# Kernel tuning notes

Measured on AMD Instinct MI355X. Metric: run time of the kernel, lower is better.

Reference implementation:

```python
import jax, jax.numpy as jnp
import numpy as np

N = 50000        # nodes
E = 800000       # edges (avg degree 16)
D_IN = 19        # in_channels(16) + 2 coords + 1 observed flag
H = 64           # graph_hidden
L = 3            # graph_layers
EPS = 1e-5       # BatchNorm eps


def setup_inputs() -> dict:
    key = jax.random.key(0)
    ks = jax.random.split(key, 12)
    s = 0.05
    x = jax.random.normal(ks[0], (N, D_IN), jnp.float32)
    edge_index = jax.random.randint(ks[1], (2, E), 0, N, dtype=jnp.int32)
    return {
        "x": x,
        "edge_index": edge_index,
        # input projection + input BN
        "w_in": jax.random.normal(ks[2], (D_IN, H), jnp.float32) * s,
        "b_in": jnp.zeros((H,), jnp.float32),
        "bn0_g": jnp.ones((H,), jnp.float32),
        "bn0_b": jnp.zeros((H,), jnp.float32),
        # per-layer SAGEConv: lin_l (aggregated neighbors, with bias), lin_r (self, no bias)
        "wl": jax.random.normal(ks[3], (L, H, H), jnp.float32) * s,
        "bl": jnp.zeros((L, H), jnp.float32),
        "wr": jax.random.normal(ks[4], (L, H, H), jnp.float32) * s,
        # per-layer BatchNorm affine
        "bn_g": jnp.ones((L, H), jnp.float32),
        "bn_b": jnp.zeros((L, H), jnp.float32),
    }


def _batchnorm(h, g, b):
    # training-mode BN over the node axis (biased variance, like torch)
    mu = h.mean(axis=0)
    var = h.var(axis=0)
    return (h - mu) * jax.lax.rsqrt(var + EPS) * g + b


def reference(x, edge_index, w_in, b_in, bn0_g, bn0_b, wl, bl, wr, bn_g, bn_b):
    src = edge_index[0]
    dst = edge_index[1]
    n = x.shape[0]

    # input_proj -> BN -> ReLU  (dropout is identity at inference)
    h = x @ w_in + b_in
    h = jax.nn.relu(_batchnorm(h, bn0_g, bn0_b))

    # in-degree for mean aggregation (computed once)
    deg = jax.ops.segment_sum(jnp.ones((src.shape[0],), h.dtype), dst, num_segments=n)
    denom = jnp.maximum(deg, 1.0)[:, None]

    for l in range(L):
        # SAGEConv(mean): gather source feats, segment-mean into targets
        msgs = h[src]                                        # [E, H] gather
        agg = jax.ops.segment_sum(msgs, dst, num_segments=n) / denom
        h_new = agg @ wl[l] + bl[l] + h @ wr[l]
        h_new = jax.nn.relu(_batchnorm(h_new, bn_g[l], bn_b[l]))
        h = h + h_new                                        # residual
    return h
```

## Files before the change

### kernel.cpp

```cpp
#include <hip/hip_runtime.h>
#include <hip/hip_bf16.h>

#define NODES 50000
#define EDGES 800000
#define DIN   19
#define LAYERS 3
#define BN_EPS 1e-5f

#define NBINS 196
#define EPB   4096
#define NBLK  196
#define NTILES 782
#define TPB   256

typedef __attribute__((ext_vector_type(4))) float f32x4;
typedef __attribute__((ext_vector_type(2))) float f32x2;
typedef __attribute__((ext_vector_type(8))) short s16x8;

__device__ inline ushort bf16bits(float f) {
    __hip_bfloat16 h = __float2bfloat16(f);
    return *reinterpret_cast<ushort*>(&h);
}

#if __has_builtin(__builtin_amdgcn_cvt_pk_f32_fp8) && __has_builtin(__builtin_amdgcn_cvt_pk_fp8_f32)
__device__ inline unsigned pack4_fp8(float a, float b, float c, float d) {
    unsigned w = __builtin_amdgcn_cvt_pk_fp8_f32(a, b, 0u, false);
    return __builtin_amdgcn_cvt_pk_fp8_f32(c, d, w, true);
}
__device__ inline void acc4_fp8(unsigned v, float& a0, float& a1, float& a2, float& a3) {
    f32x2 lo = __builtin_amdgcn_cvt_pk_f32_fp8(v, false);
    f32x2 hi = __builtin_amdgcn_cvt_pk_f32_fp8(v, true);
    a0 += lo.x; a1 += lo.y; a2 += hi.x; a3 += hi.y;
}
#else
__device__ inline unsigned enc1(float f) {
    _Float16 hf = (_Float16)f;
    unsigned u = (unsigned)*reinterpret_cast<unsigned short*>(&hf);
    u = (u + 0x7Fu + ((u >> 8) & 1u)) >> 8;
    return u & 0xFFu;
}
__device__ inline float dec1(unsigned b) {
    unsigned short u = (unsigned short)(b << 8);
    _Float16 hf = *reinterpret_cast<_Float16*>(&u);
    return (float)hf;
}
__device__ inline unsigned pack4_fp8(float a, float b, float c, float d) {
    return enc1(a) | (enc1(b) << 8) | (enc1(c) << 16) | (enc1(d) << 24);
}
__device__ inline void acc4_fp8(unsigned v, float& a0, float& a1, float& a2, float& a3) {
    a0 += dec1(v & 0xFF); a1 += dec1((v >> 8) & 0xFF);
    a2 += dec1((v >> 16) & 0xFF); a3 += dec1(v >> 24);
}
#endif


__global__ void k_wprep(const float* __restrict__ w_in, const float* __restrict__ wl,
                        const float* __restrict__ wr, ushort* __restrict__ WiT,
                        ushort* __restrict__ WcatT, int* __restrict__ bintot,
                        float* __restrict__ stats) {
    int i0 = blockIdx.x * blockDim.x + threadIdx.x;
    int stride = gridDim.x * blockDim.x;
    for (int i = i0; i < NBINS; i += stride) bintot[i] = 0;
    for (int i = i0; i < 4 * 2048; i += stride) stats[i] = 0.0f;
    for (int i = i0; i < 64 * 32; i += stride) {
        int c = i >> 5, k = i & 31;
        WiT[i] = bf16bits(k < DIN ? w_in[k * 64 + c] : 0.0f);
    }
    for (int i = i0; i < LAYERS * 64 * 128; i += stride) {
        int l = i >> 13, rem = i & 8191;
        int c = rem >> 7, k = rem & 127;
        float v = (k < 64) ? wl[(l * 64 + k) * 64 + c] : wr[(l * 64 + (k - 64)) * 64 + c];
        WcatT[i] = bf16bits(v);
    }
}


__global__ __launch_bounds__(1024) void k_sortA(const int* __restrict__ src, const int* __restrict__ dst,
                                                int2* __restrict__ cb, int* __restrict__ bintot,
                                                unsigned* __restrict__ bbuf) {
    __shared__ int hist[256];
    __shared__ int cur[256];
    __shared__ int wsum4[4];
    __shared__ unsigned stage[EPB];
    int blk = blockIdx.x, t = threadIdx.x;
    int e0 = blk * EPB;
    int ne = min(EPB, EDGES - e0);
    int d[4]; unsigned pk[4];
    #pragma unroll
    for (int i = 0; i < 4; ++i) {
        int j = t + i * 1024;
        if (j < ne) {
            int dd = dst[e0 + j];
            d[i] = dd;
            pk[i] = ((unsigned)(dd & 255) << 24) | (unsigned)src[e0 + j];
        } else d[i] = -1;
    }
    if (t < 256) hist[t] = 0;
    __syncthreads();
    #pragma unroll
    for (int i = 0; i < 4; ++i)
        if (d[i] >= 0) atomicAdd(&hist[d[i] >> 8], 1);
    __syncthreads();
    int ln = t & 63, wv = t >> 6;
    int cntv = 0, inc = 0;
    if (t < 256) {
        cntv = hist[t];
        inc = cntv;
        #pragma unroll
        for (int s = 1; s < 64; s <<= 1) {
            int u = __shfl_up(inc, s);
            if (ln >= s) inc += u;
        }
        if (ln == 63) wsum4[wv] = inc;
    }
    __syncthreads();
    if (t < 256) {
        int woff = 0;
        #pragma unroll
        for (int i = 0; i < 4; ++i) if (i < wv) woff += wsum4[i];
        int excl = woff + inc - cntv;
        cur[t] = excl;
        if (t < NBINS) {
            cb[t * NBLK + blk] = make_int2(excl, cntv);
            if (cntv) atomicAdd(&bintot[t], cntv);
        }
    }
    __syncthreads();
    #pragma unroll
    for (int i = 0; i < 4; ++i)
        if (d[i] >= 0) {
            int slot = atomicAdd(&cur[d[i] >> 8], 1);
            stage[slot] = pk[i];
        }
    __syncthreads();
    #pragma unroll
    for (int i = 0; i < 4; ++i) {
        int j = t + i * 1024;
        if (j < ne) bbuf[e0 + j] = stage[j];
    }
}


__device__ inline int ubound(const int* pre, int f) {
    int lo = 0, hi = NBLK;
    while (lo + 1 < hi) {
        int mid = (lo + hi) >> 1;
        if (pre[mid] <= f) lo = mid; else hi = mid;
    }
    return lo;
}

__global__ __launch_bounds__(TPB) void k_binB(const int2* __restrict__ cb, const int* __restrict__ bintot,
                                              const unsigned* __restrict__ bbuf,
                                              int* __restrict__ off, float* __restrict__ rden,
                                              int* __restrict__ ebuf) {
    __shared__ int red[256];
    __shared__ int segoff[NBLK], segcnt[NBLK], pre[NBLK + 1];
    __shared__ int deg[256], loff[256], cur[256];
    __shared__ int wsum4[4];
    int b = blockIdx.x, t = threadIdx.x;
    int ln = t & 63, wv = t >> 6;
    red[t] = (t < b) ? bintot[t] : 0;
    __syncthreads();
    #pragma unroll
    for (int s = 128; s > 0; s >>= 1) {
        if (t < s) red[t] += red[t + s];
        __syncthreads();
    }
    int binoff = red[0];
    if (t < NBLK) {
        int2 c = cb[b * NBLK + t];
        segoff[t] = c.x; segcnt[t] = c.y;
    }
    deg[t] = 0; cur[t] = 0;
    __syncthreads();
    if (wv == 0) {
        int carry = 0;
        for (int base = 0; base < NBLK; base += 64) {
            int idx = base + ln;
            int v = (idx < NBLK) ? segcnt[idx] : 0;
            int inc = v;
            #pragma unroll
            for (int s = 1; s < 64; s <<= 1) {
                int u = __shfl_up(inc, s);
                if (ln >= s) inc += u;
            }
            if (idx < NBLK) pre[idx] = carry + inc - v;
            carry += __shfl(inc, 63);
        }
        if (ln == 0) pre[NBLK] = carry;
    }
    __syncthreads();
    int total = pre[NBLK];
    for (int f = t; f < total; f += TPB) {
        int sg = ubound(pre, f);
        unsigned e = bbuf[sg * EPB + segoff[sg] + (f - pre[sg])];
        atomicAdd(&deg[e >> 24], 1);
    }
    __syncthreads();
    int dv = deg[t], inc2 = dv;
    #pragma unroll
    for (int s = 1; s < 64; s <<= 1) {
        int u = __shfl_up(inc2, s);
        if (ln >= s) inc2 += u;
    }
    if (ln == 63) wsum4[wv] = inc2;
    __syncthreads();
    int woff = 0;
    #pragma unroll
    for (int i = 0; i < 4; ++i) if (i < wv) woff += wsum4[i];
    int excl = woff + inc2 - dv;
    loff[t] = excl;
    int node = (b << 8) + t;
    if (node < NODES) {
        off[node] = binoff + excl;
        rden[node] = 1.0f / fmaxf((float)dv, 1.0f);
    }
    if (b == NBINS - 1 && t == 0) off[NODES] = EDGES;
    __syncthreads();
    for (int f = t; f < total; f += TPB) {
        int sg = ubound(pre, f);
        unsigned e = bbuf[sg * EPB + segoff[sg] + (f - pre[sg])];
        int dd = e >> 24;
        int slot = atomicAdd(&cur[dd], 1);
        ebuf[binoff + loff[dd] + slot] = (int)(e & 0xFFFFFFu);
    }
}


__device__ inline void gemm_epilogue(int t, int row0, f32x4* acc, const float* __restrict__ bias,
                                     ushort* __restrict__ tb, float* __restrict__ stats,
                                     float (*red)[128]) {
    int lane = t & 63, wave = t >> 6;
    int r = lane & 15, g = lane >> 4;
    float s_[4], q_[4];
    #pragma unroll
    for (int j = 0; j < 4; ++j) {
        float b = bias[j * 16 + r];
        float s = 0.0f, q = 0.0f;
        #pragma unroll
        for (int i = 0; i < 4; ++i) {
            int row = row0 + wave * 16 + g * 4 + i;
            if (row < NODES) {
                float v = acc[j][i] + b;
                tb[(size_t)row * 64 + j * 16 + r] = bf16bits(v);
                s += v; q += v * v;
            }
        }
        s += __shfl_xor(s, 16); s += __shfl_xor(s, 32);
        q += __shfl_xor(q, 16); q += __shfl_xor(q, 32);
        s_[j] = s; q_[j] = q;
    }
    if (g == 0) {
        #pragma unroll
        for (int j = 0; j < 4; ++j) {
            red[wave][j * 16 + r] = s_[j];
            red[wave][64 + j * 16 + r] = q_[j];
        }
    }
    __syncthreads();
    if (t < 128) {
        float tot = red[0][t] + red[1][t] + red[2][t] + red[3][t];
        atomicAdd(&stats[t * 16], tot);
    }
}


__global__ __launch_bounds__(TPB) void k_gemm0(const float* __restrict__ x, const ushort* __restrict__ WiT,
                                               const float* __restrict__ bias, ushort* __restrict__ tb,
                                               float* __restrict__ stats) {
    __shared__ ushort xt[64][40];
    __shared__ float red[4][128];
    int t = threadIdx.x, rb = blockIdx.x;
    int row0 = rb * 64;
    int nv = min(64, NODES - row0);
    unsigned* xz = (unsigned*)xt;
    for (int i = t; i < 64 * 20; i += TPB) xz[i] = 0;
    __syncthreads();
    const float* xs = x + (size_t)row0 * DIN;
    for (int e = t; e < nv * DIN; e += TPB) {
        int n = e / DIN, k = e - n * DIN;
        xt[n][k] = bf16bits(xs[e]);
    }
    __syncthreads();
    int lane = t & 63, wave = t >> 6;
    int r = lane & 15, g = lane >> 4;
    f32x4 acc[4] = {{0.f,0.f,0.f,0.f},{0.f,0.f,0.f,0.f},{0.f,0.f,0.f,0.f},{0.f,0.f,0.f,0.f}};
    s16x8 af = *(const s16x8*)&xt[wave * 16 + r][g * 8];
    #pragma unroll
    for (int j = 0; j < 4; ++j) {
        s16x8 bf = *(const s16x8*)(WiT + (size_t)(j * 16 + r) * 32 + g * 8);
        acc[j] = __builtin_amdgcn_mfma_f32_16x16x32_bf16(af, bf, acc[j], 0, 0, 0);
    }
    gemm_epilogue(t, row0, acc, bias, tb, stats, red);
}


__global__ __launch_bounds__(TPB) void k_gemm(const ushort* __restrict__ AB, const ushort* __restrict__ WT,
                                              const float* __restrict__ bias, ushort* __restrict__ tb,
                                              float* __restrict__ stats) {
    __shared__ float red[4][128];
    int t = threadIdx.x;
    int lane = t & 63, wave = t >> 6;
    int row0 = blockIdx.x * 64;
    int r = lane & 15, g = lane >> 4;
    f32x4 acc[4] = {{0.f,0.f,0.f,0.f},{0.f,0.f,0.f,0.f},{0.f,0.f,0.f,0.f},{0.f,0.f,0.f,0.f}};
    int ar = row0 + wave * 16 + r;
    if (ar >= NODES) ar = NODES - 1;
    #pragma unroll
    for (int k0 = 0; k0 < 128; k0 += 32) {
        s16x8 af = *(const s16x8*)(AB + (size_t)ar * 128 + k0 + g * 8);
        #pragma unroll
        for (int j = 0; j < 4; ++j) {
            s16x8 bf = *(const s16x8*)(WT + (size_t)(j * 16 + r) * 128 + k0 + g * 8);
            acc[j] = __builtin_amdgcn_mfma_f32_16x16x32_bf16(af, bf, acc[j], 0, 0, 0);
        }
    }
    gemm_epilogue(t, row0, acc, bias, tb, stats, red);
}


__global__ void k_apply(const ushort* __restrict__ tb, const float* __restrict__ stats,
                        const float* __restrict__ gamma, const float* __restrict__ beta,
                        float* __restrict__ h, ushort* __restrict__ AB,
                        unsigned* __restrict__ hb8, int residual, int write_next) {
    int idx0 = blockIdx.x * blockDim.x + threadIdx.x;
    int stride = gridDim.x * blockDim.x;
    const float invN = 1.0f / NODES;
    for (int idx = idx0; idx < NODES * 16; idx += stride) {
        int n = idx >> 4;
        int j = (idx & 15) * 4;
        ushort4 tv = *(const ushort4*)(tb + (size_t)n * 64 + j);
        float tf[4] = { __uint_as_float((unsigned)tv.x << 16), __uint_as_float((unsigned)tv.y << 16),
                        __uint_as_float((unsigned)tv.z << 16), __uint_as_float((unsigned)tv.w << 16) };
        f32x4 hv;
        if (residual) hv = *(const f32x4*)(h + (size_t)n * 64 + j);
        float out[4];
        ushort ub[4];
        #pragma unroll
        for (int k = 0; k < 4; ++k) {
            int f = j + k;
            float mu = stats[f * 16] * invN;
            float var = stats[(64 + f) * 16] * invN - mu * mu;
            float sc = gamma[f] * rsqrtf(var + BN_EPS);
            float sh = beta[f] - mu * sc;
            float v = fmaxf(tf[k] * sc + sh, 0.0f);
            out[k] = residual ? (hv[k] + v) : v;
            ub[k] = bf16bits(out[k]);
        }
        *(f32x4*)(h + (size_t)n * 64 + j) = f32x4{out[0], out[1], out[2], out[3]};
        if (write_next) {
            *(ushort4*)(AB + (size_t)n * 128 + 64 + j) = make_ushort4(ub[0], ub[1], ub[2], ub[3]);
            hb8[(size_t)n * 16 + (idx & 15)] = pack4_fp8(out[0], out[1], out[2], out[3]);
        }
    }
}


__global__ void k_agg(const int* __restrict__ off, const int* __restrict__ ebuf,
                      const float* __restrict__ rden, const unsigned* __restrict__ hb8,
                      ushort* __restrict__ ABh) {
    unsigned* AB = (unsigned*)ABh;
    int t = threadIdx.x;
    int lane = t & 63;
    int q = lane >> 4;
    int fl = lane & 15;
    int w = blockIdx.x * (blockDim.x >> 6) + (t >> 6);
    int nw = gridDim.x * (blockDim.x >> 6);
    for (int n = w; n < NODES; n += nw) {
        int p0 = off[n], p1 = off[n + 1];
        float a0 = 0.f, a1 = 0.f, a2 = 0.f, a3 = 0.f;
        int p = p0 + q;
        for (; p + 12 < p1; p += 16) {
            int s0 = ebuf[p], s1 = ebuf[p + 4], s2 = ebuf[p + 8], s3 = ebuf[p + 12];
            unsigned v0 = hb8[(size_t)s0 * 16 + fl];
            unsigned v1 = hb8[(size_t)s1 * 16 + fl];
            unsigned v2 = hb8[(size_t)s2 * 16 + fl];
            unsigned v3 = hb8[(size_t)s3 * 16 + fl];
            acc4_fp8(v0, a0, a1, a2, a3);
            acc4_fp8(v1, a0, a1, a2, a3);
            acc4_fp8(v2, a0, a1, a2, a3);
            acc4_fp8(v3, a0, a1, a2, a3);
        }
        for (; p < p1; p += 4) {
            unsigned v = hb8[(size_t)ebuf[p] * 16 + fl];
            acc4_fp8(v, a0, a1, a2, a3);
        }
        a0 += __shfl_xor(a0, 16); a0 += __shfl_xor(a0, 32);
        a1 += __shfl_xor(a1, 16); a1 += __shfl_xor(a1, 32);
        a2 += __shfl_xor(a2, 16); a2 += __shfl_xor(a2, 32);
        a3 += __shfl_xor(a3, 16); a3 += __shfl_xor(a3, 32);
        if (q == 0) {
            float rd = rden[n];
            uint2 o;
            o.x = (unsigned)bf16bits(a0 * rd) | ((unsigned)bf16bits(a1 * rd) << 16);
            o.y = (unsigned)bf16bits(a2 * rd) | ((unsigned)bf16bits(a3 * rd) << 16);
            *(uint2*)(AB + (size_t)n * 64 + fl * 2) = o;
        }
    }
}


extern "C" void kernel_launch(void* const* d_in, const int* in_sizes, int n_in,
                              void* d_out, int out_size, void* d_ws, size_t ws_size,
                              hipStream_t stream) {
    const float* x    = (const float*)d_in[0];
    const int*   ei   = (const int*)d_in[1];
    const float* w_in = (const float*)d_in[2];
    const float* b_in = (const float*)d_in[3];
    const float* bn0g = (const float*)d_in[4];
    const float* bn0b = (const float*)d_in[5];
    const float* wl   = (const float*)d_in[6];
    const float* bl   = (const float*)d_in[7];
    const float* wr   = (const float*)d_in[8];
    const float* bng  = (const float*)d_in[9];
    const float* bnb  = (const float*)d_in[10];
    const int* esrc = ei;
    const int* edst = ei + EDGES;
    float* h = (float*)d_out;

    char* p = (char*)d_ws;
    auto alloc = [&](size_t bytes) {
        char* r = p;
        p += (bytes + 255) & ~size_t(255);
        return r;
    };
    int*      bintot = (int*)alloc((size_t)NBINS * 4);
    float*    stats  = (float*)alloc((size_t)4 * 2048 * 4);
    int2*     cb     = (int2*)alloc((size_t)NBINS * NBLK * 8);
    unsigned* bbuf   = (unsigned*)alloc((size_t)NBLK * EPB * 4);
    int*      off    = (int*)alloc((size_t)(NODES + 1) * 4);
    float*    rden   = (float*)alloc((size_t)NODES * 4);
    int*      ebuf   = (int*)alloc((size_t)EDGES * 4);
    ushort*   WiT    = (ushort*)alloc(64 * 32 * 2);
    ushort*   WcatT  = (ushort*)alloc(LAYERS * 64 * 128 * 2);
    ushort*   tb     = (ushort*)alloc((size_t)NODES * 64 * 2);
    ushort*   AB     = (ushort*)alloc((size_t)NODES * 128 * 2);
    unsigned* hb8    = (unsigned*)alloc((size_t)NODES * 16 * 4);

    k_wprep<<<128, TPB, 0, stream>>>(w_in, wl, wr, WiT, WcatT, bintot, stats);
    k_sortA<<<NBLK, 1024, 0, stream>>>(esrc, edst, cb, bintot, bbuf);
    k_binB<<<NBINS, TPB, 0, stream>>>(cb, bintot, bbuf, off, rden, ebuf);

    k_gemm0<<<NTILES, TPB, 0, stream>>>(x, WiT, b_in, tb, stats);
    k_apply<<<2048, TPB, 0, stream>>>(tb, stats, bn0g, bn0b, h, AB, hb8, 0, 1);

    for (int l = 0; l < LAYERS; ++l) {
        k_agg<<<2048, TPB, 0, stream>>>(off, ebuf, rden, hb8, AB);
        k_gemm<<<NTILES, TPB, 0, stream>>>(AB, WcatT + l * 8192, bl + l * 64,
                                           tb, stats + (l + 1) * 2048);
        k_apply<<<2048, TPB, 0, stream>>>(tb, stats + (l + 1) * 2048, bng + l * 64, bnb + l * 64,
                                          h, AB, hb8, 1, l < LAYERS - 1 ? 1 : 0);
    }
}
```

Before: 295.2 us.

## Co-schedule edge sort with input GEMM and CSR build with BN0 apply

```diff
diff --git a/kernel.cpp b/kernel.cpp
--- a/kernel.cpp
+++ b/kernel.cpp
@@ -11,6 +11,8 @@
 #define EPB   4096
 #define NBLK  196
 #define NTILES 782
+#define G0TILES 196
+#define APPLY_BLOCKS 2048
 #define TPB   256
 
 typedef __attribute__((ext_vector_type(4))) float f32x4;
@@ -54,10 +56,10 @@
 #endif
 
 
-__global__ void k_wprep(const float* __restrict__ w_in, const float* __restrict__ wl,
-                        const float* __restrict__ wr, ushort* __restrict__ WiT,
-                        ushort* __restrict__ WcatT, int* __restrict__ bintot,
-                        float* __restrict__ stats) {
+__global__ void k_prep(const float* __restrict__ w_in, const float* __restrict__ wl,
+                       const float* __restrict__ wr, ushort* __restrict__ WiT,
+                       ushort* __restrict__ WcatT, int* __restrict__ bintot,
+                       float* __restrict__ stats) {
     int i0 = blockIdx.x * blockDim.x + threadIdx.x;
     int stride = gridDim.x * blockDim.x;
     for (int i = i0; i < NBINS; i += stride) bintot[i] = 0;
@@ -75,14 +77,15 @@
 }
 
 
-__global__ __launch_bounds__(1024) void k_sortA(const int* __restrict__ src, const int* __restrict__ dst,
-                                                int2* __restrict__ cb, int* __restrict__ bintot,
-                                                unsigned* __restrict__ bbuf) {
-    __shared__ int hist[256];
-    __shared__ int cur[256];
-    __shared__ int wsum4[4];
-    __shared__ unsigned stage[EPB];
-    int blk = blockIdx.x, t = threadIdx.x;
+union SMemK2 {
+    struct { int hist[256], cur[256], wsum[4]; unsigned stage[EPB]; } sort;
+    struct { ushort xt[256][40]; float red[4][4][128]; } g0;
+};
+
+__device__ inline void do_sortA(int blk, int t, const int* __restrict__ src,
+                                const int* __restrict__ dst, int2* __restrict__ cb,
+                                int* __restrict__ bintot, unsigned* __restrict__ bbuf,
+                                SMemK2& sm) {
     int e0 = blk * EPB;
     int ne = min(EPB, EDGES - e0);
     int d[4]; unsigned pk[4];
@@ -95,31 +98,31 @@
             pk[i] = ((unsigned)(dd & 255) << 24) | (unsigned)src[e0 + j];
         } else d[i] = -1;
     }
-    if (t < 256) hist[t] = 0;
+    if (t < 256) sm.sort.hist[t] = 0;
     __syncthreads();
     #pragma unroll
     for (int i = 0; i < 4; ++i)
-        if (d[i] >= 0) atomicAdd(&hist[d[i] >> 8], 1);
+        if (d[i] >= 0) atomicAdd(&sm.sort.hist[d[i] >> 8], 1);
     __syncthreads();
     int ln = t & 63, wv = t >> 6;
     int cntv = 0, inc = 0;
     if (t < 256) {
-        cntv = hist[t];
+        cntv = sm.sort.hist[t];
         inc = cntv;
         #pragma unroll
         for (int s = 1; s < 64; s <<= 1) {
             int u = __shfl_up(inc, s);
             if (ln >= s) inc += u;
         }
-        if (ln == 63) wsum4[wv] = inc;
+        if (ln == 63) sm.sort.wsum[wv] = inc;
     }
     __syncthreads();
     if (t < 256) {
         int woff = 0;
         #pragma unroll
-        for (int i = 0; i < 4; ++i) if (i < wv) woff += wsum4[i];
+        for (int i = 0; i < 4; ++i) if (i < wv) woff += sm.sort.wsum[i];
         int excl = woff + inc - cntv;
-        cur[t] = excl;
+        sm.sort.cur[t] = excl;
         if (t < NBINS) {
             cb[t * NBLK + blk] = make_int2(excl, cntv);
             if (cntv) atomicAdd(&bintot[t], cntv);
@@ -129,15 +132,86 @@
     #pragma unroll
     for (int i = 0; i < 4; ++i)
         if (d[i] >= 0) {
-            int slot = atomicAdd(&cur[d[i] >> 8], 1);
-            stage[slot] = pk[i];
+            int slot = atomicAdd(&sm.sort.cur[d[i] >> 8], 1);
+            sm.sort.stage[slot] = pk[i];
         }
     __syncthreads();
     #pragma unroll
     for (int i = 0; i < 4; ++i) {
         int j = t + i * 1024;
-        if (j < ne) bbuf[e0 + j] = stage[j];
-    }
+        if (j < ne) bbuf[e0 + j] = sm.sort.stage[j];
+    }
+}
+
+__device__ inline void do_gemm0(int tile, int t, const float* __restrict__ x,
+                                const ushort* __restrict__ WiT, const float* __restrict__ bias,
+                                ushort* __restrict__ tb, float* __restrict__ stats,
+                                SMemK2& sm) {
+    int base = tile * 256;
+    int nv = min(256, NODES - base);
+    unsigned* xz = (unsigned*)sm.g0.xt;
+    for (int i = t; i < 256 * 20; i += 1024) xz[i] = 0;
+    __syncthreads();
+    const float* xs = x + (size_t)base * DIN;
+    for (int e = t; e < nv * DIN; e += 1024) {
+        int n = e / DIN, k = e - n * DIN;
+        sm.g0.xt[n][k] = bf16bits(xs[e]);
+    }
+    __syncthreads();
+    int grp = t >> 8, tl = t & 255;
+    int lane = t & 63, wl = (tl >> 6);
+    int r = lane & 15, g = lane >> 4;
+    f32x4 acc[4] = {{0.f,0.f,0.f,0.f},{0.f,0.f,0.f,0.f},{0.f,0.f,0.f,0.f},{0.f,0.f,0.f,0.f}};
+    s16x8 af = *(const s16x8*)&sm.g0.xt[grp * 64 + wl * 16 + r][g * 8];
+    #pragma unroll
+    for (int j = 0; j < 4; ++j) {
+        s16x8 bf = *(const s16x8*)(WiT + (size_t)(j * 16 + r) * 32 + g * 8);
+        acc[j] = __builtin_amdgcn_mfma_f32_16x16x32_bf16(af, bf, acc[j], 0, 0, 0);
+    }
+    int row0 = base + grp * 64 + wl * 16;
+    float s_[4], q_[4];
+    #pragma unroll
+    for (int j = 0; j < 4; ++j) {
+        float b = bias[j * 16 + r];
+        float s = 0.0f, q = 0.0f;
+        #pragma unroll
+        for (int i = 0; i < 4; ++i) {
+            int row = row0 + g * 4 + i;
+            if (row < NODES) {
+                float v = acc[j][i] + b;
+                tb[(size_t)row * 64 + j * 16 + r] = bf16bits(v);
+                s += v; q += v * v;
+            }
+        }
+        s += __shfl_xor(s, 16); s += __shfl_xor(s, 32);
+        q += __shfl_xor(q, 16); q += __shfl_xor(q, 32);
+        s_[j] = s; q_[j] = q;
+    }
+    if (g == 0) {
+        #pragma unroll
+        for (int j = 0; j < 4; ++j) {
+            sm.g0.red[grp][wl][j * 16 + r] = s_[j];
+            sm.g0.red[grp][wl][64 + j * 16 + r] = q_[j];
+        }
+    }
+    __syncthreads();
+    if (tl < 128) {
+        float tot = sm.g0.red[grp][0][tl] + sm.g0.red[grp][1][tl] +
+                    sm.g0.red[grp][2][tl] + sm.g0.red[grp][3][tl];
+        atomicAdd(&stats[tl * 16], tot);
+    }
+}
+
+__global__ __launch_bounds__(1024) void k_sort_g0(const int* __restrict__ esrc, const int* __restrict__ edst,
+                                                  int2* __restrict__ cb, int* __restrict__ bintot,
+                                                  unsigned* __restrict__ bbuf,
+                                                  const float* __restrict__ x, const ushort* __restrict__ WiT,
+                                                  const float* __restrict__ bias, ushort* __restrict__ tb,
+                                                  float* __restrict__ stats) {
+    __shared__ SMemK2 sm;
+    int t = threadIdx.x;
+    if (blockIdx.x < NBLK) do_sortA(blockIdx.x, t, esrc, edst, cb, bintot, bbuf, sm);
+    else                   do_gemm0(blockIdx.x - NBLK, t, x, WiT, bias, tb, stats, sm);
 }
 
 
@@ -150,67 +224,69 @@
     return lo;
 }
 
-__global__ __launch_bounds__(TPB) void k_binB(const int2* __restrict__ cb, const int* __restrict__ bintot,
-                                              const unsigned* __restrict__ bbuf,
-                                              int* __restrict__ off, float* __restrict__ rden,
-                                              int* __restrict__ ebuf) {
-    __shared__ int red[256];
-    __shared__ int segoff[NBLK], segcnt[NBLK], pre[NBLK + 1];
-    __shared__ int deg[256], loff[256], cur[256];
-    __shared__ int wsum4[4];
-    int b = blockIdx.x, t = threadIdx.x;
+struct SMemBinB {
+    int red[256];
+    int segoff[NBLK], segcnt[NBLK], pre[NBLK + 1];
+    int deg[256], loff[256], cur[256];
+    int wsum4[4];
+};
+
+__device__ inline void do_binB(int b, int t, const int2* __restrict__ cb,
+                               const int* __restrict__ bintot, const unsigned* __restrict__ bbuf,
+                               int* __restrict__ off, float* __restrict__ rden,
+                               int* __restrict__ ebuf, SMemBinB& sm) {
     int ln = t & 63, wv = t >> 6;
-    red[t] = (t < b) ? bintot[t] : 0;
+    sm.red[t] = (t < b) ? bintot[t] : 0;
     __syncthreads();
     #pragma unroll
     for (int s = 128; s > 0; s >>= 1) {
-        if (t < s) red[t] += red[t + s];
+        if (t < s) sm.red[t] += sm.red[t + s];
         __syncthreads();
     }
-    int binoff = red[0];
+    int binoff = sm.red[0];
     if (t < NBLK) {
         int2 c = cb[b * NBLK + t];
-        segoff[t] = c.x; segcnt[t] = c.y;
-    }
-    deg[t] = 0; cur[t] = 0;
+        sm.segoff[t] = c.x; sm.segcnt[t] = c.y;
+    }
+    sm.deg[t] = 0; sm.cur[t] = 0;
     __syncthreads();
     if (wv == 0) {
         int carry = 0;
         for (int base = 0; base < NBLK; base += 64) {
             int idx = base + ln;
-            int v = (idx < NBLK) ? segcnt[idx] : 0;
+            int v = (idx < NBLK) ? sm.segcnt[idx] : 0;
             int inc = v;
             #pragma unroll
             for (int s = 1; s < 64; s <<= 1) {
                 int u = __shfl_up(inc, s);
                 if (ln >= s) inc += u;
             }
-            if (idx < NBLK) pre[idx] = carry + inc - v;
+            if (idx < NBLK) sm.pre[idx] = carry + inc - v;
             carry += __shfl(inc, 63);
         }
-        if (ln == 0) pre[NBLK] = carry;
-    }
-    __syncthreads();
-    int total = pre[NBLK];
+        if (ln == 0) sm.pre[NBLK] = carry;
+    }
+    __syncthreads();
+    int total = sm.pre[NBLK];
     for (int f = t; f < total; f += TPB) {
-        int sg = ubound(pre, f);
-        unsigned e = bbuf[sg * EPB + segoff[sg] + (f - pre[sg])];
-        atomicAdd(&deg[e >> 24], 1);
-    }
-    __syncthreads();
-    int dv = deg[t], inc2 = dv;
+        int sg = ubound(sm.pre, f);
+        unsigned e = bbuf[sg * EPB + sm.segoff[sg] + (f - sm.pre[sg])];
+        atomicAdd(&sm.deg[e >> 24], 1);
+    }
+    __syncthreads();
+    int dv = sm.deg[t], inc2 = dv;
     #pragma unroll
     for (int s = 1; s < 64; s <<= 1) {
         int u = __shfl_up(inc2, s);
         if (ln >= s) inc2 += u;
     }
-    if (ln == 63) wsum4[wv] = inc2;
+    if (ln == 63) sm.wsum4[wv] = inc2;
     __syncthreads();
     int woff = 0;
     #pragma unroll
-    for (int i = 0; i < 4; ++i) if (i < wv) woff += wsum4[i];
+    for (int i = 0; i < 4; ++i) if (i < wv) woff += sm.wsum4[i];
     int excl = woff + inc2 - dv;
-    loff[t] = excl;
+    sm.loff[t] = excl;
     int node = (b << 8) + t;
     if (node < NODES) {
         off[node] = binoff + excl;
@@ -219,80 +295,65 @@
     if (b == NBINS - 1 && t == 0) off[NODES] = EDGES;
     __syncthreads();
     for (int f = t; f < total; f += TPB) {
-        int sg = ubound(pre, f);
-        unsigned e = bbuf[sg * EPB + segoff[sg] + (f - pre[sg])];
+        int sg = ubound(sm.pre, f);
+        unsigned e = bbuf[sg * EPB + sm.segoff[sg] + (f - sm.pre[sg])];
         int dd = e >> 24;
-        int slot = atomicAdd(&cur[dd], 1);
-        ebuf[binoff + loff[dd] + slot] = (int)(e & 0xFFFFFFu);
-    }
-}
-
-
-__device__ inline void gemm_epilogue(int t, int row0, f32x4* acc, const float* __restrict__ bias,
-                                     ushort* __restrict__ tb, float* __restrict__ stats,
-                                     float (*red)[128]) {
-    int lane = t & 63, wave = t >> 6;
-    int r = lane & 15, g = lane >> 4;
-    float s_[4], q_[4];
-    #pragma unroll
-    for (int j = 0; j < 4; ++j) {
-        float b = bias[j * 16 + r];
-        float s = 0.0f, q = 0.0f;
-        #pragma unroll
-        for (int i = 0; i < 4; ++i) {
-            int row = row0 + wave * 16 + g * 4 + i;
-            if (row < NODES) {
-                float v = acc[j][i] + b;
-                tb[(size_t)row * 64 + j * 16 + r] = bf16bits(v);
-                s += v; q += v * v;
-            }
-        }
-        s += __shfl_xor(s, 16); s += __shfl_xor(s, 32);
-        q += __shfl_xor(q, 16); q += __shfl_xor(q, 32);
-        s_[j] = s; q_[j] = q;
-    }
-    if (g == 0) {
-        #pragma unroll
-        for (int j = 0; j < 4; ++j) {
-            red[wave][j * 16 + r] = s_[j];
-            red[wave][64 + j * 16 + r] = q_[j];
-        }
-    }
-    __syncthreads();
-    if (t < 128) {
-        float tot = red[0][t] + red[1][t] + red[2][t] + red[3][t];
-        atomicAdd(&stats[t * 16], tot);
-    }
-}
-
-
-__global__ __launch_bounds__(TPB) void k_gemm0(const float* __restrict__ x, const ushort* __restrict__ WiT,
-                                               const float* __restrict__ bias, ushort* __restrict__ tb,
-                                               float* __restrict__ stats) {
-    __shared__ ushort xt[64][40];
-    __shared__ float red[4][128];
-    int t = threadIdx.x, rb = blockIdx.x;
-    int row0 = rb * 64;
-    int nv = min(64, NODES - row0);
-    unsigned* xz = (unsigned*)xt;
-    for (int i = t; i < 64 * 20; i += TPB) xz[i] = 0;
-    __syncthreads();
-    const float* xs = x + (size_t)row0 * DIN;
-    for (int e = t; e < nv * DIN; e += TPB) {
-        int n = e / DIN, k = e - n * DIN;
-        xt[n][k] = bf16bits(xs[e]);
-    }
-    __syncthreads();
-    int lane = t & 63, wave = t >> 6;
-    int r = lane & 15, g = lane >> 4;
-    f32x4 acc[4] = {{0.f,0.f,0.f,0.f},{0.f,0.f,0.f,0.f},{0.f,0.f,0.f,0.f},{0.f,0.f,0.f,0.f}};
-    s16x8 af = *(const s16x8*)&xt[wave * 16 + r][g * 8];
-    #pragma unroll
-    for (int j = 0; j < 4; ++j) {
-        s16x8 bf = *(const s16x8*)(WiT + (size_t)(j * 16 + r) * 32 + g * 8);
-        acc[j] = __builtin_amdgcn_mfma_f32_16x16x32_bf16(af, bf, acc[j], 0, 0, 0);
-    }
-    gemm_epilogue(t, row0, acc, bias, tb, stats, red);
+        int slot = atomicAdd(&sm.cur[dd], 1);
+        ebuf[binoff + sm.loff[dd] + slot] = (int)(e & 0xFFFFFFu);
+    }
+}
+
+__device__ inline void do_apply(int idx0, int stride, const ushort* __restrict__ tb,
+                                const float* __restrict__ stats, const float* __restrict__ gamma,
+                                const float* __restrict__ beta, float* __restrict__ h,
+                                ushort* __restrict__ AB, unsigned* __restrict__ hb8,
+                                int residual, int write_next) {
+    const float invN = 1.0f / NODES;
+    for (int idx = idx0; idx < NODES * 16; idx += stride) {
+        int n = idx >> 4;
+        int j = (idx & 15) * 4;
+        ushort4 tv = *(const ushort4*)(tb + (size_t)n * 64 + j);
+        float tf[4] = { __uint_as_float((unsigned)tv.x << 16), __uint_as_float((unsigned)tv.y << 16),
+                        __uint_as_float((unsigned)tv.z << 16), __uint_as_float((unsigned)tv.w << 16) };
+        f32x4 hv;
+        if (residual) hv = *(const f32x4*)(h + (size_t)n * 64 + j);
+        float out[4];
+        ushort ub[4];
+        #pragma unroll
+        for (int k = 0; k < 4; ++k) {
+            int f = j + k;
+            float mu = stats[f * 16] * invN;
+            float var = stats[(64 + f) * 16] * invN - mu * mu;
+            float sc = gamma[f] * rsqrtf(var + BN_EPS);
+            float sh = beta[f] - mu * sc;
+            float v = fmaxf(tf[k] * sc + sh, 0.0f);
+            out[k] = residual ? (hv[k] + v) : v;
+            ub[k] = bf16bits(out[k]);
+        }
+        *(f32x4*)(h + (size_t)n * 64 + j) = f32x4{out[0], out[1], out[2], out[3]};
+        if (write_next) {
+            *(ushort4*)(AB + (size_t)n * 128 + 64 + j) = make_ushort4(ub[0], ub[1], ub[2], ub[3]);
+            hb8[(size_t)n * 16 + (idx & 15)] = pack4_fp8(out[0], out[1], out[2], out[3]);
+        }
+    }
+}
+
+__global__ __launch_bounds__(TPB) void k_csr_bn0(const int2* __restrict__ cb, const int* __restrict__ bintot,
+                                                 const unsigned* __restrict__ bbuf,
+                                                 int* __restrict__ off, float* __restrict__ rden,
+                                                 int* __restrict__ ebuf,
+                                                 const ushort* __restrict__ tb, const float* __restrict__ stats,
+                                                 const float* __restrict__ gamma, const float* __restrict__ beta,
+                                                 float* __restrict__ h, ushort* __restrict__ AB,
+                                                 unsigned* __restrict__ hb8) {
+    __shared__ SMemBinB sm;
+    int t = threadIdx.x;
+    if (blockIdx.x < NBINS) {
+        do_binB(blockIdx.x, t, cb, bintot, bbuf, off, rden, ebuf, sm);
+    } else {
+        int vb = blockIdx.x - NBINS;
+        do_apply(vb * TPB + t, APPLY_BLOCKS * TPB, tb, stats, gamma, beta, h, AB, hb8, 0, 1);
+    }
 }
 
 
@@ -316,7 +377,36 @@
             acc[j] = __builtin_amdgcn_mfma_f32_16x16x32_bf16(af, bf, acc[j], 0, 0, 0);
         }
     }
-    gemm_epilogue(t, row0, acc, bias, tb, stats, red);
+    float s_[4], q_[4];
+    #pragma unroll
+    for (int j = 0; j < 4; ++j) {
+        float b = bias[j * 16 + r];
+        float s = 0.0f, q = 0.0f;
+        #pragma unroll
+        for (int i = 0; i < 4; ++i) {
+            int row = row0 + wave * 16 + g * 4 + i;
+            if (row < NODES) {
+                float v = acc[j][i] + b;
+                tb[(size_t)row * 64 + j * 16 + r] = bf16bits(v);
+                s += v; q += v * v;
+            }
+        }
+        s += __shfl_xor(s, 16); s += __shfl_xor(s, 32);
+        q += __shfl_xor(q, 16); q += __shfl_xor(q, 32);
+        s_[j] = s; q_[j] = q;
+    }
+    if (g == 0) {
+        #pragma unroll
+        for (int j = 0; j < 4; ++j) {
+            red[wave][j * 16 + r] = s_[j];
+            red[wave][64 + j * 16 + r] = q_[j];
+        }
+    }
+    __syncthreads();
+    if (t < 128) {
+        float tot = red[0][t] + red[1][t] + red[2][t] + red[3][t];
+        atomicAdd(&stats[t * 16], tot);
+    }
 }
 
 
@@ -324,36 +414,8 @@
                         const float* __restrict__ gamma, const float* __restrict__ beta,
                         float* __restrict__ h, ushort* __restrict__ AB,
                         unsigned* __restrict__ hb8, int residual, int write_next) {
-    int idx0 = blockIdx.x * blockDim.x + threadIdx.x;
-    int stride = gridDim.x * blockDim.x;
-    const float invN = 1.0f / NODES;
-    for (int idx = idx0; idx < NODES * 16; idx += stride) {
-        int n = idx >> 4;
-        int j = (idx & 15) * 4;
-        ushort4 tv = *(const ushort4*)(tb + (size_t)n * 64 + j);
-        float tf[4] = { __uint_as_float((unsigned)tv.x << 16), __uint_as_float((unsigned)tv.y << 16),
-                        __uint_as_float((unsigned)tv.z << 16), __uint_as_float((unsigned)tv.w << 16) };
-        f32x4 hv;
-        if (residual) hv = *(const f32x4*)(h + (size_t)n * 64 + j);
-        float out[4];
-        ushort ub[4];
-        #pragma unroll
-        for (int k = 0; k < 4; ++k) {
-            int f = j + k;
-            float mu = stats[f * 16] * invN;
-            float var = stats[(64 + f) * 16] * invN - mu * mu;
-            float sc = gamma[f] * rsqrtf(var + BN_EPS);
-            float sh = beta[f] - mu * sc;
-            float v = fmaxf(tf[k] * sc + sh, 0.0f);
-            out[k] = residual ? (hv[k] + v) : v;
-            ub[k] = bf16bits(out[k]);
-        }
-        *(f32x4*)(h + (size_t)n * 64 + j) = f32x4{out[0], out[1], out[2], out[3]};
-        if (write_next) {
-            *(ushort4*)(AB + (size_t)n * 128 + 64 + j) = make_ushort4(ub[0], ub[1], ub[2], ub[3]);
-            hb8[(size_t)n * 16 + (idx & 15)] = pack4_fp8(out[0], out[1], out[2], out[3]);
-        }
-    }
+    do_apply(blockIdx.x * blockDim.x + threadIdx.x, gridDim.x * blockDim.x,
+             tb, stats, gamma, beta, h, AB, hb8, residual, write_next);
 }
 
 
@@ -438,18 +500,18 @@
     ushort*   AB     = (ushort*)alloc((size_t)NODES * 128 * 2);
     unsigned* hb8    = (unsigned*)alloc((size_t)NODES * 16 * 4);
 
-    k_wprep<<<128, TPB, 0, stream>>>(w_in, wl, wr, WiT, WcatT, bintot, stats);
-    k_sortA<<<NBLK, 1024, 0, stream>>>(esrc, edst, cb, bintot, bbuf);
-    k_binB<<<NBINS, TPB, 0, stream>>>(cb, bintot, bbuf, off, rden, ebuf);
-
-    k_gemm0<<<NTILES, TPB, 0, stream>>>(x, WiT, b_in, tb, stats);
-    k_apply<<<2048, TPB, 0, stream>>>(tb, stats, bn0g, bn0b, h, AB, hb8, 0, 1);
+    k_prep<<<128, TPB, 0, stream>>>(w_in, wl, wr, WiT, WcatT, bintot, stats);
+    k_sort_g0<<<NBLK + G0TILES, 1024, 0, stream>>>(esrc, edst, cb, bintot, bbuf,
+                                                   x, WiT, b_in, tb, stats);
+    k_csr_bn0<<<NBINS + APPLY_BLOCKS, TPB, 0, stream>>>(cb, bintot, bbuf, off, rden, ebuf,
+                                                        tb, stats, bn0g, bn0b, h, AB, hb8);
 
     for (int l = 0; l < LAYERS; ++l) {
         k_agg<<<2048, TPB, 0, stream>>>(off, ebuf, rden, hb8, AB);
         k_gemm<<<NTILES, TPB, 0, stream>>>(AB, WcatT + l * 8192, bl + l * 64,
                                            tb, stats + (l + 1) * 2048);
-        k_apply<<<2048, TPB, 0, stream>>>(tb, stats + (l + 1) * 2048, bng + l * 64, bnb + l * 64,
-                                          h, AB, hb8, 1, l < LAYERS - 1 ? 1 : 0);
-    }
-}
+        k_apply<<<APPLY_BLOCKS, TPB, 0, stream>>>(tb, stats + (l + 1) * 2048, bng + l * 64,
+                                                  bnb + l * 64, h, AB, hb8, 1,
+                                                  l < LAYERS - 1 ? 1 : 0);
+    }
+}
```

Result: faster. 279.1 us (-5.5%).
